# Kernel tuning notes

Measured on AMD Instinct MI355X. Metric: run time of the kernel, lower is better.

Reference implementation:

```python
import jax, jax.numpy as jnp
import numpy as np

HID, HEADS, LAYERS, EDIM = 128, 2, 3, 1
HEAD_DIM = HID  # out_channels per head (concat=False -> mean over heads)
N_NODES, N_EDGES = 50000, 500000
LN_EPS = 1e-5


def _layer_norm(x, g, b):
    mu = x.mean(-1, keepdims=True)
    var = ((x - mu) ** 2).mean(-1, keepdims=True)
    return (x - mu) * jax.lax.rsqrt(var + LN_EPS) * g + b


def _transformer_conv(x, src, tgt, edge_attr, Wq, bq, Wk, bk, Wv, bv, We, Wskip, bskip):
    # PyG TransformerConv, concat=False, root_weight=True, lin_edge bias=False
    N = x.shape[0]
    E = src.shape[0]
    q = (x @ Wq + bq).reshape(N, HEADS, HEAD_DIM)
    k = (x @ Wk + bk).reshape(N, HEADS, HEAD_DIM)
    v = (x @ Wv + bv).reshape(N, HEADS, HEAD_DIM)
    e = (edge_attr @ We).reshape(E, HEADS, HEAD_DIM)          # [E,H,C]
    k_j = k[src] + e                                          # gather + edge bias
    q_i = q[tgt]
    alpha = (q_i * k_j).sum(-1) / jnp.sqrt(jnp.asarray(HEAD_DIM, x.dtype))  # [E,H]
    # scatter-softmax over incoming edges of each target node
    m = jax.ops.segment_max(alpha, tgt, num_segments=N)       # [N,H]
    a = jnp.exp(alpha - m[tgt])
    denom = jax.ops.segment_sum(a, tgt, num_segments=N)
    a = a / jnp.where(denom[tgt] > 0, denom[tgt], 1.0)
    msg = (v[src] + e) * a[..., None]                         # [E,H,C]
    out = jax.ops.segment_sum(msg, tgt, num_segments=N)       # [N,H,C]
    out = out.mean(axis=1)                                    # concat=False -> head mean
    return out + x @ Wskip + bskip                            # root/skip connection


def reference(x, edge_index, edge_attr, ln_in_g, ln_in_b,
              Wq, bq, Wk, bk, Wv, bv, We, Wskip, bskip, ln_g, ln_b):
    src, tgt = edge_index[0], edge_index[1]
    x = _layer_norm(x, ln_in_g, ln_in_b)
    for l in range(LAYERS):
        h = _transformer_conv(x, src, tgt, edge_attr,
                              Wq[l], bq[l], Wk[l], bk[l], Wv[l], bv[l],
                              We[l], Wskip[l], bskip[l])
        h = jax.nn.elu(h)
        x = _layer_norm(x + h, ln_g[l], ln_b[l])
    return x


def setup_inputs() -> dict:
    key = jax.random.key(0)
    ks = jax.random.split(key, 12)
    HC = HEADS * HEAD_DIM
    s = 1.0 / np.sqrt(HID)
    inp = {
        "x": jax.random.normal(ks[0], (N_NODES, HID), jnp.float32),
        "edge_index": jax.random.randint(ks[1], (2, N_EDGES), 0, N_NODES, jnp.int64),
        "edge_attr": jax.random.normal(ks[2], (N_EDGES, EDIM), jnp.float32),
        "ln_in_g": jnp.ones((HID,), jnp.float32),
        "ln_in_b": jnp.zeros((HID,), jnp.float32),
        "Wq": jax.random.normal(ks[3], (LAYERS, HID, HC), jnp.float32) * s,
        "bq": jnp.zeros((LAYERS, HC), jnp.float32),
        "Wk": jax.random.normal(ks[4], (LAYERS, HID, HC), jnp.float32) * s,
        "bk": jnp.zeros((LAYERS, HC), jnp.float32),
        "Wv": jax.random.normal(ks[5], (LAYERS, HID, HC), jnp.float32) * s,
        "bv": jnp.zeros((LAYERS, HC), jnp.float32),
        "We": jax.random.normal(ks[6], (LAYERS, EDIM, HC), jnp.float32),
        "Wskip": jax.random.normal(ks[7], (LAYERS, HID, HID), jnp.float32) * s,
        "bskip": jnp.zeros((LAYERS, HID), jnp.float32),
        "ln_g": jnp.ones((LAYERS, HID), jnp.float32),
        "ln_b": jnp.zeros((LAYERS, HID), jnp.float32),
    }
    return inp
```

## Files before the change

kernel.cpp:

```cpp
#include <hip/hip_runtime.h>
#include <math.h>

#define NN 50000
#define NE 500000
#define HIDS 128
#define MCOLS 896
#define NLAYERS 3

typedef __attribute__((ext_vector_type(8))) short short8;
typedef __attribute__((ext_vector_type(4))) float floatx4;
typedef _Float16 half8v __attribute__((ext_vector_type(8)));

#define STR 152

static __device__ __forceinline__ unsigned short f2bf(float f) {
    unsigned u = __float_as_uint(f);
    u += 0x7fffu + ((u >> 16) & 1u);
    return (unsigned short)(u >> 16);
}
static __device__ __forceinline__ unsigned short f2h(float f) {
    union { _Float16 h; unsigned short u; } c;
    c.h = (_Float16)f;
    return c.u;
}
#define DPP_ADD(v, ctrl) \
    v += __int_as_float(__builtin_amdgcn_mov_dpp(__float_as_int(v), ctrl, 0xf, 0xf, true))
static __device__ __forceinline__ float wred16(float v) {
    DPP_ADD(v, 0xB1);
    DPP_ADD(v, 0x4E);
    DPP_ADD(v, 0x124);
    DPP_ADD(v, 0x128);
    return v;
}
static __device__ __forceinline__ float wred64(float v) {
    v += __shfl_xor(v, 1, 64);
    v += __shfl_xor(v, 2, 64);
    v += __shfl_xor(v, 4, 64);
    v += __shfl_xor(v, 8, 64);
    v += __shfl_xor(v, 16, 64);
    v += __shfl_xor(v, 32, 64);
    return v;
}

__global__ __launch_bounds__(256) void eatb_count(const int* __restrict__ tgt, int* __restrict__ cnt) {
    int e = blockIdx.x * 256 + threadIdx.x;
    if (e < NE) atomicAdd(&cnt[tgt[e]], 1);
}

__global__ __launch_bounds__(256) void eatb_blocksum(const int* __restrict__ cnt, int* __restrict__ bsums) {
    __shared__ int sm[256];
    int i = blockIdx.x * 256 + threadIdx.x;
    sm[threadIdx.x] = (i < NN) ? cnt[i] : 0;
    __syncthreads();
    for (int off = 128; off > 0; off >>= 1) {
        if (threadIdx.x < off) sm[threadIdx.x] += sm[threadIdx.x + off];
        __syncthreads();
    }
    if (threadIdx.x == 0) bsums[blockIdx.x] = sm[0];
}

__global__ __launch_bounds__(256) void eatb_scanb(int* __restrict__ bsums, int nb) {
    __shared__ int sm[256];
    int t = threadIdx.x;
    int v = (t < nb) ? bsums[t] : 0;
    sm[t] = v;
    __syncthreads();
    for (int off = 1; off < 256; off <<= 1) {
        int x = (t >= off) ? sm[t - off] : 0;
        __syncthreads();
        sm[t] += x;
        __syncthreads();
    }
    if (t < nb) bsums[t] = sm[t] - v;
}

__global__ __launch_bounds__(256) void eatb_rowstart(const int* __restrict__ cnt, const int* __restrict__ bsums,
                                                     int* __restrict__ row_start) {
    __shared__ int sm[256];
    int t = threadIdx.x;
    int i = blockIdx.x * 256 + t;
    int v = (i < NN) ? cnt[i] : 0;
    sm[t] = v;
    __syncthreads();
    for (int off = 1; off < 256; off <<= 1) {
        int x = (t >= off) ? sm[t - off] : 0;
        __syncthreads();
        sm[t] += x;
        __syncthreads();
    }
    int excl = sm[t] - v + bsums[blockIdx.x];
    if (i < NN) row_start[i] = excl;
    if (i == NN - 1) row_start[NN] = excl + v;
}

__global__ __launch_bounds__(256) void eatb_scatter(const int* __restrict__ src, const int* __restrict__ tgt,
                                                    const float* __restrict__ ea, const int* __restrict__ row_start,
                                                    int* __restrict__ cursor, int2* __restrict__ csr) {
    int e = blockIdx.x * 256 + threadIdx.x;
    if (e >= NE) return;
    int t = tgt[e];
    int pos = atomicAdd(&cursor[t], 1);
    int2 val;
    val.x = src[e];
    val.y = __float_as_int(ea[e]);
    csr[row_start[t] + pos] = val;
}

__global__ __launch_bounds__(256) void eatb_packw(const float* __restrict__ Wq, const float* __restrict__ Wk,
                                                  const float* __restrict__ Wv, const float* __restrict__ Ws,
                                                  const float* __restrict__ bq, const float* __restrict__ bk,
                                                  const float* __restrict__ bv, const float* __restrict__ bs,
                                                  unsigned short* __restrict__ Wt, float* __restrict__ bcat) {
    int idx = blockIdx.x * 256 + threadIdx.x;
    const int WTOT = NLAYERS * MCOLS * HIDS;
    if (idx < WTOT) {
        int l = idx / (MCOLS * HIDS);
        int rem = idx % (MCOLS * HIDS);
        int c = rem / HIDS, k = rem % HIDS;
        float v;
        if (c < 256)      v = Wq[(l * HIDS + k) * 256 + c];
        else if (c < 512) v = Wk[(l * HIDS + k) * 256 + c - 256];
        else if (c < 768) v = Wv[(l * HIDS + k) * 256 + c - 512];
        else              v = Ws[(l * HIDS + k) * 128 + c - 768];
        Wt[idx] = f2bf(v);
    } else {
        int i2 = idx - WTOT;
        if (i2 < NLAYERS * MCOLS) {
            int l = i2 / MCOLS, c = i2 % MCOLS;
            float v;
            if (c < 256)      v = bq[l * 256 + c];
            else if (c < 512) v = bk[l * 256 + c - 256];
            else if (c < 768) v = bv[l * 256 + c - 512];
            else              v = bs[l * 128 + c - 768];
            bcat[i2] = v;
        }
    }
}

__global__ __launch_bounds__(256) void eatb_ln_in(const float* __restrict__ x, const float* __restrict__ g,
                                                  const float* __restrict__ b, float* __restrict__ xout,
                                                  unsigned short* __restrict__ xb) {
    int wid = threadIdx.x >> 6, lane = threadIdx.x & 63;
    int n = blockIdx.x * 4 + wid;
    if (n >= NN) return;
    float2 v = *(const float2*)(x + (size_t)n * HIDS + 2 * lane);
    float mu = wred64(v.x + v.y) * (1.f / 128.f);
    float cx = v.x - mu, cy = v.y - mu;
    float var = wred64(cx * cx + cy * cy) * (1.f / 128.f);
    float r = rsqrtf(var + 1e-5f);
    float2 g2 = *(const float2*)(g + 2 * lane);
    float2 b2 = *(const float2*)(b + 2 * lane);
    float2 o;
    o.x = cx * r * g2.x + b2.x;
    o.y = cy * r * g2.y + b2.y;
    *(float2*)(xout + (size_t)n * HIDS + 2 * lane) = o;
    unsigned pk = (unsigned)f2bf(o.x) | ((unsigned)f2bf(o.y) << 16);
    *(unsigned*)(xb + (size_t)n * HIDS + 2 * lane) = pk;
}

__global__ __launch_bounds__(512, 1) void eatb_gemm(const unsigned short* __restrict__ xb,
                                                    const unsigned short* __restrict__ Wt,
                                                    const float* __restrict__ bias,
                                                    unsigned short* __restrict__ qpack,
                                                    unsigned short* __restrict__ kvpack,
                                                    float* __restrict__ skipbuf) {
    __shared__ __align__(16) char smem[2 * 128 * STR * 2];
    short* As = (short*)smem;
    short* Bs = As + 128 * STR;
    float* Cs = (float*)smem;

    int tid = threadIdx.x;
    int r0 = blockIdx.x * 128;
    int c0 = blockIdx.y * 128;

    {
        int row = tid >> 4, ch = (tid & 15) * 8;
        #pragma unroll
        for (int p = 0; p < 4; ++p) {
            int r = row + p * 32;
            int gr = r0 + r;
            uint4 v = make_uint4(0, 0, 0, 0);
            if (gr < NN) v = *(const uint4*)(xb + (size_t)gr * HIDS + ch);
            *(uint4*)(As + r * STR + ch) = v;
        }
        #pragma unroll
        for (int p = 0; p < 4; ++p) {
            int r = row + p * 32;
            uint4 v = *(const uint4*)(Wt + (size_t)(c0 + r) * HIDS + ch);
            *(uint4*)(Bs + r * STR + ch) = v;
        }
    }
    __syncthreads();

    int wid = tid >> 6, lane = tid & 63;
    int fr = lane & 15;
    int kq = (lane >> 4) * 8;
    floatx4 acc[8] = {};
    #pragma unroll
    for (int ks = 0; ks < 4; ++ks) {
        int kof = ks * 32 + kq;
        short8 af = *(const short8*)(As + (wid * 16 + fr) * STR + kof);
        #pragma unroll
        for (int n = 0; n < 8; ++n) {
            short8 bf = *(const short8*)(Bs + (n * 16 + fr) * STR + kof);
            acc[n] = __builtin_amdgcn_mfma_f32_16x16x32_bf16(af, bf, acc[n], 0, 0, 0);
        }
    }
    __syncthreads();
    #pragma unroll
    for (int ni = 0; ni < 8; ++ni)
        #pragma unroll
        for (int rg = 0; rg < 4; ++rg) {
            int rr = wid * 16 + (lane >> 4) * 4 + rg;
            Cs[rr * 129 + ni * 16 + fr] = acc[ni][rg];
        }
    __syncthreads();

    int cl = (tid & 31) * 4;
    int C = c0 + cl;
    float4 b4 = *(const float4*)(bias + C);
    #pragma unroll
    for (int p = 0; p < 8; ++p) {
        int rr = (tid >> 5) + 16 * p;
        int gr = r0 + rr;
        if (gr >= NN) break;
        float v0 = Cs[rr * 129 + cl] + b4.x;
        float v1 = Cs[rr * 129 + cl + 1] + b4.y;
        float v2 = Cs[rr * 129 + cl + 2] + b4.z;
        float v3 = Cs[rr * 129 + cl + 3] + b4.w;
        if (C < 256) {
            ushort4 o;
            o.x = f2h(v0); o.y = f2h(v1); o.z = f2h(v2); o.w = f2h(v3);
            *(ushort4*)(qpack + (size_t)gr * 256 + C) = o;
        } else if (C < 768) {
            int u = C - 256;
            int part = u >> 7;
            int h = part & 1, isv = part >> 1;
            int d0 = u & 127;
            ushort4 o;
            o.x = f2h(v0); o.y = f2h(v1); o.z = f2h(v2); o.w = f2h(v3);
            size_t off = (size_t)gr * 512 + ((h * 16 + (d0 >> 3)) * 16) + isv * 8 + (d0 & 7);
            *(ushort4*)(kvpack + off) = o;
        } else {
            *(float4*)(skipbuf + (size_t)gr * 128 + (C - 768)) = make_float4(v0, v1, v2, v3);
        }
    }
}

__global__ __launch_bounds__(256) void eatb_attn(const unsigned short* __restrict__ qpack,
                                                 const unsigned short* __restrict__ kvpack,
                                                 const float* __restrict__ skipbuf,
                                                 const int2* __restrict__ csr, const int* __restrict__ row_start,
                                                 const float* __restrict__ Wel, const float* __restrict__ g,
                                                 const float* __restrict__ beta, const float* __restrict__ xcur,
                                                 float* __restrict__ dst, unsigned short* __restrict__ xbout) {
    int wid = threadIdx.x >> 6;
    int lane = threadIdx.x & 63;
    int n = blockIdx.x * 4 + wid;
    if (n >= NN) return;
    int slot = lane >> 5;
    int h = (lane >> 4) & 1;
    int sl = lane & 15;
    int dbase = sl * 8;

    const float rs = 0.08838834764831845f;
    const _Float16* qh16 = (const _Float16*)qpack;
    const _Float16* kvh = (const _Float16*)kvpack;

    half8v qh = *(const half8v*)(qh16 + n * 256 + h * 128 + dbase);
    float q0 = (float)qh[0] * rs, q1 = (float)qh[1] * rs, q2 = (float)qh[2] * rs, q3 = (float)qh[3] * rs;
    float q4 = (float)qh[4] * rs, q5 = (float)qh[5] * rs, q6 = (float)qh[6] * rs, q7 = (float)qh[7] * rs;
    const float* wep = Wel + h * 128 + dbase;
    float4 wea = *(const float4*)wep;
    float4 web = *(const float4*)(wep + 4);
    float qwe = wred16(q0 * wea.x + q1 * wea.y + q2 * wea.z + q3 * wea.w +
                       q4 * web.x + q5 * web.y + q6 * web.z + q7 * web.w);

    float sA = 0.f, seaA = 0.f, sB = 0.f, seaB = 0.f;
    float aA0 = 0.f, aA1 = 0.f, aA2 = 0.f, aA3 = 0.f, aA4 = 0.f, aA5 = 0.f, aA6 = 0.f, aA7 = 0.f;
    float aB0 = 0.f, aB1 = 0.f, aB2 = 0.f, aB3 = 0.f, aB4 = 0.f, aB5 = 0.f, aB6 = 0.f, aB7 = 0.f;
    int beg = row_start[n], end = row_start[n + 1];
    int nit = (end - beg + 3) >> 2;
    int lbase = (h * 16 + sl) << 4;
    for (int it = 0; it < nit; ++it) {
        int eA = beg + 4 * it + slot;
        int eB = eA + 2;
        bool vA = eA < end, vB = eB < end;
        int2 seA = csr[vA ? eA : beg];
        int2 seB = csr[vB ? eB : beg];
        int koA = (seA.x << 9) + lbase;
        int koB = (seB.x << 9) + lbase;
        half8v kqA = *(const half8v*)(kvh + koA);
        half8v vqA = *(const half8v*)(kvh + koA + 8);
        half8v kqB = *(const half8v*)(kvh + koB);
        half8v vqB = *(const half8v*)(kvh + koB + 8);
        float eaA = __int_as_float(seA.y);
        float eaB = __int_as_float(seB.y);
        float pA = q0 * (float)kqA[0] + q1 * (float)kqA[1] + q2 * (float)kqA[2] + q3 * (float)kqA[3] +
                   q4 * (float)kqA[4] + q5 * (float)kqA[5] + q6 * (float)kqA[6] + q7 * (float)kqA[7];
        float pB = q0 * (float)kqB[0] + q1 * (float)kqB[1] + q2 * (float)kqB[2] + q3 * (float)kqB[3] +
                   q4 * (float)kqB[4] + q5 * (float)kqB[5] + q6 * (float)kqB[6] + q7 * (float)kqB[7];
        pA = wred16(pA);
        pB = wred16(pB);
        float wA = vA ? __expf(pA + eaA * qwe) : 0.f;
        float wB = vB ? __expf(pB + eaB * qwe) : 0.f;
        sA += wA;
        sB += wB;
        seaA = fmaf(wA, eaA, seaA);
        seaB = fmaf(wB, eaB, seaB);
        aA0 = fmaf(wA, (float)vqA[0], aA0);  aB0 = fmaf(wB, (float)vqB[0], aB0);
        aA1 = fmaf(wA, (float)vqA[1], aA1);  aB1 = fmaf(wB, (float)vqB[1], aB1);
        aA2 = fmaf(wA, (float)vqA[2], aA2);  aB2 = fmaf(wB, (float)vqB[2], aB2);
        aA3 = fmaf(wA, (float)vqA[3], aA3);  aB3 = fmaf(wB, (float)vqB[3], aB3);
        aA4 = fmaf(wA, (float)vqA[4], aA4);  aB4 = fmaf(wB, (float)vqB[4], aB4);
        aA5 = fmaf(wA, (float)vqA[5], aA5);  aB5 = fmaf(wB, (float)vqB[5], aB5);
        aA6 = fmaf(wA, (float)vqA[6], aA6);  aB6 = fmaf(wB, (float)vqB[6], aB6);
        aA7 = fmaf(wA, (float)vqA[7], aA7);  aB7 = fmaf(wB, (float)vqB[7], aB7);
    }
    float s = sA + sB, sea = seaA + seaB;
    float a0 = aA0 + aB0, a1 = aA1 + aB1, a2 = aA2 + aB2, a3 = aA3 + aB3;
    float a4 = aA4 + aB4, a5 = aA5 + aB5, a6 = aA6 + aB6, a7 = aA7 + aB7;

    s += __shfl_xor(s, 32, 64);
    sea += __shfl_xor(sea, 32, 64);
    a0 += __shfl_xor(a0, 32, 64);
    a1 += __shfl_xor(a1, 32, 64);
    a2 += __shfl_xor(a2, 32, 64);
    a3 += __shfl_xor(a3, 32, 64);
    a4 += __shfl_xor(a4, 32, 64);
    a5 += __shfl_xor(a5, 32, 64);
    a6 += __shfl_xor(a6, 32, 64);
    a7 += __shfl_xor(a7, 32, 64);

    float inv = (s > 0.f) ? 1.f / s : 1.f;
    float sw = sea * inv;
    float o0 = a0 * inv + sw * wea.x;
    float o1 = a1 * inv + sw * wea.y;
    float o2 = a2 * inv + sw * wea.z;
    float o3 = a3 * inv + sw * wea.w;
    float o4 = a4 * inv + sw * web.x;
    float o5 = a5 * inv + sw * web.y;
    float o6 = a6 * inv + sw * web.z;
    float o7 = a7 * inv + sw * web.w;
    o0 = 0.5f * (o0 + __shfl_xor(o0, 16, 64));
    o1 = 0.5f * (o1 + __shfl_xor(o1, 16, 64));
    o2 = 0.5f * (o2 + __shfl_xor(o2, 16, 64));
    o3 = 0.5f * (o3 + __shfl_xor(o3, 16, 64));
    o4 = 0.5f * (o4 + __shfl_xor(o4, 16, 64));
    o5 = 0.5f * (o5 + __shfl_xor(o5, 16, 64));
    o6 = 0.5f * (o6 + __shfl_xor(o6, 16, 64));
    o7 = 0.5f * (o7 + __shfl_xor(o7, 16, 64));

    const float* skp = skipbuf + n * 128 + dbase;
    const float* xrp = xcur + n * 128 + dbase;
    float4 ska = *(const float4*)skp, skb = *(const float4*)(skp + 4);
    float4 xra = *(const float4*)xrp, xrb = *(const float4*)(xrp + 4);
    float y0 = o0 + ska.x, y1 = o1 + ska.y, y2 = o2 + ska.z, y3 = o3 + ska.w;
    float y4 = o4 + skb.x, y5 = o5 + skb.y, y6 = o6 + skb.z, y7 = o7 + skb.w;
    y0 = (y0 > 0.f) ? y0 : __expf(y0) - 1.f;
    y1 = (y1 > 0.f) ? y1 : __expf(y1) - 1.f;
    y2 = (y2 > 0.f) ? y2 : __expf(y2) - 1.f;
    y3 = (y3 > 0.f) ? y3 : __expf(y3) - 1.f;
    y4 = (y4 > 0.f) ? y4 : __expf(y4) - 1.f;
    y5 = (y5 > 0.f) ? y5 : __expf(y5) - 1.f;
    y6 = (y6 > 0.f) ? y6 : __expf(y6) - 1.f;
    y7 = (y7 > 0.f) ? y7 : __expf(y7) - 1.f;
    float p0 = xra.x + y0, p1 = xra.y + y1, p2 = xra.z + y2, p3 = xra.w + y3;
    float p4 = xrb.x + y4, p5 = xrb.y + y5, p6 = xrb.z + y6, p7 = xrb.w + y7;
    float mu = wred16(p0 + p1 + p2 + p3 + p4 + p5 + p6 + p7) * (1.f / 128.f);
    float c0 = p0 - mu, c1 = p1 - mu, c2 = p2 - mu, c3 = p3 - mu;
    float c4 = p4 - mu, c5 = p5 - mu, c6 = p6 - mu, c7 = p7 - mu;
    float var = wred16(c0 * c0 + c1 * c1 + c2 * c2 + c3 * c3 +
                       c4 * c4 + c5 * c5 + c6 * c6 + c7 * c7) * (1.f / 128.f);
    float r = rsqrtf(var + 1e-5f);
    if (lane < 16) {
        const float* gp = g + dbase;
        const float* bp = beta + dbase;
        float4 ga = *(const float4*)gp, gb = *(const float4*)(gp + 4);
        float4 ba = *(const float4*)bp, bb = *(const float4*)(bp + 4);
        float4 oa, ob;
        oa.x = c0 * r * ga.x + ba.x; oa.y = c1 * r * ga.y + ba.y;
        oa.z = c2 * r * ga.z + ba.z; oa.w = c3 * r * ga.w + ba.w;
        ob.x = c4 * r * gb.x + bb.x; ob.y = c5 * r * gb.y + bb.y;
        ob.z = c6 * r * gb.z + bb.z; ob.w = c7 * r * gb.w + bb.w;
        float* dp = dst + n * 128 + dbase;
        *(float4*)dp = oa;
        *(float4*)(dp + 4) = ob;
        if (xbout) {
            uint4 pk;
            pk.x = (unsigned)f2bf(oa.x) | ((unsigned)f2bf(oa.y) << 16);
            pk.y = (unsigned)f2bf(oa.z) | ((unsigned)f2bf(oa.w) << 16);
            pk.z = (unsigned)f2bf(ob.x) | ((unsigned)f2bf(ob.y) << 16);
            pk.w = (unsigned)f2bf(ob.z) | ((unsigned)f2bf(ob.w) << 16);
            *(uint4*)(xbout + n * 128 + dbase) = pk;
        }
    }
}

extern "C" void kernel_launch(void* const* d_in, const int* in_sizes, int n_in,
                              void* d_out, int out_size, void* d_ws, size_t ws_size,
                              hipStream_t stream) {
    const float* x       = (const float*)d_in[0];
    const int*   ei      = (const int*)d_in[1];
    const float* eattr   = (const float*)d_in[2];
    const float* ln_in_g = (const float*)d_in[3];
    const float* ln_in_b = (const float*)d_in[4];
    const float* Wq = (const float*)d_in[5];
    const float* bq = (const float*)d_in[6];
    const float* Wk = (const float*)d_in[7];
    const float* bk = (const float*)d_in[8];
    const float* Wv = (const float*)d_in[9];
    const float* bv = (const float*)d_in[10];
    const float* We = (const float*)d_in[11];
    const float* Ws = (const float*)d_in[12];
    const float* bs = (const float*)d_in[13];
    const float* ln_g = (const float*)d_in[14];
    const float* ln_b = (const float*)d_in[15];
    float* out = (float*)d_out;

    char* p = (char*)d_ws;
    auto carve = [&](size_t bytes) {
        char* r = p;
        p += (bytes + 255) & ~(size_t)255;
        return (void*)r;
    };
    int*  cursor    = (int*)carve((size_t)NN * 4);
    int*  row_start = (int*)carve((size_t)(NN + 1) * 4);
    int*  bsums     = (int*)carve(1024);
    int2* csr       = (int2*)carve((size_t)NE * 8);
    unsigned short* WcatT = (unsigned short*)carve((size_t)NLAYERS * MCOLS * HIDS * 2);
    float* bcat     = (float*)carve((size_t)NLAYERS * MCOLS * 4);
    float* xcur     = (float*)carve((size_t)NN * HIDS * 4);
    unsigned short* qpack  = (unsigned short*)carve((size_t)NN * 256 * 2);
    unsigned short* kvpack = (unsigned short*)carve((size_t)NN * 512 * 2);
    float* skipbuf  = (float*)carve((size_t)NN * HIDS * 4);
    unsigned short* xb = (unsigned short*)carve((size_t)NN * HIDS * 2);

    const int NB_N = (NN + 255) / 256;
    const int NB_E = (NE + 255) / 256;
    const int NODE_BLOCKS = (NN + 3) / 4;

    hipMemsetAsync(cursor, 0, (size_t)NN * 4, stream);
    eatb_count<<<NB_E, 256, 0, stream>>>(ei + NE, cursor);
    eatb_blocksum<<<NB_N, 256, 0, stream>>>(cursor, bsums);
    eatb_scanb<<<1, 256, 0, stream>>>(bsums, NB_N);
    eatb_rowstart<<<NB_N, 256, 0, stream>>>(cursor, bsums, row_start);
    hipMemsetAsync(cursor, 0, (size_t)NN * 4, stream);
    eatb_scatter<<<NB_E, 256, 0, stream>>>(ei, ei + NE, eattr, row_start, cursor, csr);

    {
        int tot = NLAYERS * MCOLS * HIDS + NLAYERS * MCOLS;
        eatb_packw<<<(tot + 255) / 256, 256, 0, stream>>>(Wq, Wk, Wv, Ws, bq, bk, bv, bs, WcatT, bcat);
    }

    eatb_ln_in<<<NODE_BLOCKS, 256, 0, stream>>>(x, ln_in_g, ln_in_b, xcur, xb);

    dim3 ggrid((NN + 127) / 128, MCOLS / 128);
    for (int l = 0; l < NLAYERS; ++l) {
        eatb_gemm<<<ggrid, 512, 0, stream>>>(xb, WcatT + (size_t)l * MCOLS * HIDS, bcat + (size_t)l * MCOLS,
                                             qpack, kvpack, skipbuf);
        float* dst = (l == NLAYERS - 1) ? out : xcur;
        unsigned short* xbo = (l == NLAYERS - 1) ? nullptr : xb;
        eatb_attn<<<NODE_BLOCKS, 256, 0, stream>>>(qpack, kvpack, skipbuf, csr, row_start,
                                                   We + (size_t)l * 256, ln_g + (size_t)l * 128,
                                                   ln_b + (size_t)l * 128, xcur, dst, xbo);
    }
    (void)in_sizes; (void)n_in; (void)out_size; (void)ws_size;
}
```

Baseline: 576.2 us.

## Restructure GEMM to keep A tile resident and loop over column chunks

```diff
diff --git a/kernel.cpp b/kernel.cpp
--- a/kernel.cpp
+++ b/kernel.cpp
@@ -11,7 +11,7 @@
 typedef __attribute__((ext_vector_type(4))) float floatx4;
 typedef _Float16 half8v __attribute__((ext_vector_type(8)));
 
-#define STR 152
+#define GSTR 144
 
 static __device__ __forceinline__ unsigned short f2bf(float f) {
     unsigned u = __float_as_uint(f);
@@ -158,92 +158,96 @@
     *(unsigned*)(xb + (size_t)n * HIDS + 2 * lane) = pk;
 }
 
-__global__ __launch_bounds__(512, 1) void eatb_gemm(const unsigned short* __restrict__ xb,
+__global__ __launch_bounds__(256, 3) void eatb_gemm(const unsigned short* __restrict__ xb,
                                                     const unsigned short* __restrict__ Wt,
                                                     const float* __restrict__ bias,
                                                     unsigned short* __restrict__ qpack,
                                                     unsigned short* __restrict__ kvpack,
                                                     float* __restrict__ skipbuf) {
-    __shared__ __align__(16) char smem[2 * 128 * STR * 2];
-    short* As = (short*)smem;
-    short* Bs = As + 128 * STR;
-    float* Cs = (float*)smem;
+    __shared__ __align__(16) short As[64 * GSTR];
+    __shared__ __align__(16) short Bs[64 * GSTR];
+    __shared__ __align__(16) float Cs[64 * 65];
 
     int tid = threadIdx.x;
-    int r0 = blockIdx.x * 128;
-    int c0 = blockIdx.y * 128;
-
-    {
-        int row = tid >> 4, ch = (tid & 15) * 8;
-        #pragma unroll
-        for (int p = 0; p < 4; ++p) {
-            int r = row + p * 32;
-            int gr = r0 + r;
-            uint4 v = make_uint4(0, 0, 0, 0);
-            if (gr < NN) v = *(const uint4*)(xb + (size_t)gr * HIDS + ch);
-            *(uint4*)(As + r * STR + ch) = v;
-        }
-        #pragma unroll
-        for (int p = 0; p < 4; ++p) {
-            int r = row + p * 32;
-            uint4 v = *(const uint4*)(Wt + (size_t)(c0 + r) * HIDS + ch);
-            *(uint4*)(Bs + r * STR + ch) = v;
-        }
+    int r0 = blockIdx.x * 64;
+    int row = tid >> 4, ch = (tid & 15) * 8;
+
+    #pragma unroll
+    for (int p = 0; p < 4; ++p) {
+        int r = row + p * 16;
+        int gr = r0 + r;
+        uint4 v = make_uint4(0, 0, 0, 0);
+        if (gr < NN) v = *(const uint4*)(xb + (size_t)gr * HIDS + ch);
+        *(uint4*)(As + r * GSTR + ch) = v;
+    }
+    #pragma unroll
+    for (int p = 0; p < 4; ++p) {
+        int r = row + p * 16;
+        *(uint4*)(Bs + r * GSTR + ch) = *(const uint4*)(Wt + (size_t)r * HIDS + ch);
     }
     __syncthreads();
 
     int wid = tid >> 6, lane = tid & 63;
     int fr = lane & 15;
     int kq = (lane >> 4) * 8;
-    floatx4 acc[8] = {};
-    #pragma unroll
-    for (int ks = 0; ks < 4; ++ks) {
-        int kof = ks * 32 + kq;
-        short8 af = *(const short8*)(As + (wid * 16 + fr) * STR + kof);
+
+    for (int ci = 0; ci < 14; ++ci) {
+        floatx4 acc[4] = {};
         #pragma unroll
-        for (int n = 0; n < 8; ++n) {
-            short8 bf = *(const short8*)(Bs + (n * 16 + fr) * STR + kof);
-            acc[n] = __builtin_amdgcn_mfma_f32_16x16x32_bf16(af, bf, acc[n], 0, 0, 0);
+        for (int ks = 0; ks < 4; ++ks) {
+            int kof = ks * 32 + kq;
+            short8 af = *(const short8*)(As + (wid * 16 + fr) * GSTR + kof);
+            #pragma unroll
+            for (int n = 0; n < 4; ++n) {
+                short8 bf = *(const short8*)(Bs + (n * 16 + fr) * GSTR + kof);
+                acc[n] = __builtin_amdgcn_mfma_f32_16x16x32_bf16(af, bf, acc[n], 0, 0, 0);
+            }
         }
-    }
-    __syncthreads();
-    #pragma unroll
-    for (int ni = 0; ni < 8; ++ni)
         #pragma unroll
-        for (int rg = 0; rg < 4; ++rg) {
-            int rr = wid * 16 + (lane >> 4) * 4 + rg;
-            Cs[rr * 129 + ni * 16 + fr] = acc[ni][rg];
+        for (int n = 0; n < 4; ++n)
+            #pragma unroll
+            for (int rg = 0; rg < 4; ++rg)
+                Cs[(wid * 16 + (lane >> 4) * 4 + rg) * 65 + n * 16 + fr] = acc[n][rg];
+        __syncthreads();
+
+        int c0 = ci * 64;
+        int cl = (tid & 15) * 4;
+        int C = c0 + cl;
+        float4 b4 = *(const float4*)(bias + C);
+        #pragma unroll
+        for (int p = 0; p < 4; ++p) {
+            int rr = (tid >> 4) + 16 * p;
+            int gr = r0 + rr;
+            if (gr >= NN) break;
+            float v0 = Cs[rr * 65 + cl] + b4.x;
+            float v1 = Cs[rr * 65 + cl + 1] + b4.y;
+            float v2 = Cs[rr * 65 + cl + 2] + b4.z;
+            float v3 = Cs[rr * 65 + cl + 3] + b4.w;
+            if (C < 256) {
+                ushort4 o;
+                o.x = f2h(v0); o.y = f2h(v1); o.z = f2h(v2); o.w = f2h(v3);
+                *(ushort4*)(qpack + (size_t)gr * 256 + C) = o;
+            } else if (C < 768) {
+                int u = C - 256;
+                int part = u >> 7;
+                int h = part & 1, isv = part >> 1;
+                int d0 = u & 127;
+                ushort4 o;
+                o.x = f2h(v0); o.y = f2h(v1); o.z = f2h(v2); o.w = f2h(v3);
+                size_t off = (size_t)gr * 512 + ((h * 16 + (d0 >> 3)) * 16) + isv * 8 + (d0 & 7);
+                *(ushort4*)(kvpack + off) = o;
+            } else {
+                *(float4*)(skipbuf + (size_t)gr * 128 + (C - 768)) = make_float4(v0, v1, v2, v3);
+            }
         }
-    __syncthreads();
-
-    int cl = (tid & 31) * 4;
-    int C = c0 + cl;
-    float4 b4 = *(const float4*)(bias + C);
-    #pragma unroll
-    for (int p = 0; p < 8; ++p) {
-        int rr = (tid >> 5) + 16 * p;
-        int gr = r0 + rr;
-        if (gr >= NN) break;
-        float v0 = Cs[rr * 129 + cl] + b4.x;
-        float v1 = Cs[rr * 129 + cl + 1] + b4.y;
-        float v2 = Cs[rr * 129 + cl + 2] + b4.z;
-        float v3 = Cs[rr * 129 + cl + 3] + b4.w;
-        if (C < 256) {
-            ushort4 o;
-            o.x = f2h(v0); o.y = f2h(v1); o.z = f2h(v2); o.w = f2h(v3);
-            *(ushort4*)(qpack + (size_t)gr * 256 + C) = o;
-        } else if (C < 768) {
-            int u = C - 256;
-            int part = u >> 7;
-            int h = part & 1, isv = part >> 1;
-            int d0 = u & 127;
-            ushort4 o;
-            o.x = f2h(v0); o.y = f2h(v1); o.z = f2h(v2); o.w = f2h(v3);
-            size_t off = (size_t)gr * 512 + ((h * 16 + (d0 >> 3)) * 16) + isv * 8 + (d0 & 7);
-            *(ushort4*)(kvpack + off) = o;
-        } else {
-            *(float4*)(skipbuf + (size_t)gr * 128 + (C - 768)) = make_float4(v0, v1, v2, v3);
+        if (ci < 13) {
+            #pragma unroll
+            for (int p = 0; p < 4; ++p) {
+                int r = row + p * 16;
+                *(uint4*)(Bs + r * GSTR + ch) = *(const uint4*)(Wt + (size_t)((ci + 1) * 64 + r) * HIDS + ch);
+            }
         }
+        __syncthreads();
     }
 }
 
@@ -455,10 +459,10 @@
 
     eatb_ln_in<<<NODE_BLOCKS, 256, 0, stream>>>(x, ln_in_g, ln_in_b, xcur, xb);
 
-    dim3 ggrid((NN + 127) / 128, MCOLS / 128);
+    const int GEMM_BLOCKS = (NN + 63) / 64;
     for (int l = 0; l < NLAYERS; ++l) {
-        eatb_gemm<<<ggrid, 512, 0, stream>>>(xb, WcatT + (size_t)l * MCOLS * HIDS, bcat + (size_t)l * MCOLS,
-                                             qpack, kvpack, skipbuf);
+        eatb_gemm<<<GEMM_BLOCKS, 256, 0, stream>>>(xb, WcatT + (size_t)l * MCOLS * HIDS,
+                                                   bcat + (size_t)l * MCOLS, qpack, kvpack, skipbuf);
         float* dst = (l == NLAYERS - 1) ? out : xcur;
         unsigned short* xbo = (l == NLAYERS - 1) ? nullptr : xb;
         eatb_attn<<<NODE_BLOCKS, 256, 0, stream>>>(qpack, kvpack, skipbuf, csr, row_start,
```

Result: slower. 589.6 us (+2.3%).
